# Performance work log

Hardware: AMD Instinct MI355X
Metric: run time of the kernel (lower is better)

The kernel has to match this reference:

```python
import jax, jax.numpy as jnp
import numpy as np

R, T, M, N, L = 128, 4096, 32768, 4096, 16384
ALPHA_LO, ALPHA_HI = 0.01, 1.0
BETA_LO, BETA_HI = 1.0, 8.0


def setup_inputs() -> dict:
    key = jax.random.key(0)
    ks = jax.random.split(key, 7)
    x = jax.random.normal(ks[0], (R, T), dtype=jnp.float32)          # route flows param
    A = jax.random.uniform(ks[1], (M, R), dtype=jnp.float32)          # route->movement incidence
    t0 = jax.random.uniform(ks[2], (L,), dtype=jnp.float32) * 10.0    # free-flow time per c_df row
    cap = jax.random.uniform(ks[3], (L,), dtype=jnp.float32) * 1000.0 + 500.0  # capacity
    radio = jax.random.uniform(ks[4], (L,), dtype=jnp.float32)
    node_ids = jax.random.randint(ks[5], (M,), 0, N, dtype=jnp.int32)  # node of each movement row
    row_node = jax.random.randint(ks[6], (L,), 0, N, dtype=jnp.int32)  # node of each c_df row
    # logit((0.15-0.01)/0.99) and logit((4-1)/7) anchors
    alpha_raw = jnp.float32(np.log(0.141414 / (1 - 0.141414)))
    beta_raw = jnp.float32(np.log((3.0 / 7.0) / (1 - 3.0 / 7.0)))
    return {"x": x, "A": A, "t0": t0, "cap": cap, "radio": radio,
            "alpha_raw": alpha_raw, "beta_raw": beta_raw,
            "node_ids": node_ids, "row_node": row_node}


def reference(x, A, t0, cap, radio, alpha_raw, beta_raw, node_ids, row_node):
    alpha = ALPHA_LO + (ALPHA_HI - ALPHA_LO) * jax.nn.sigmoid(alpha_raw)
    beta = BETA_LO + (BETA_HI - BETA_LO) * jax.nn.sigmoid(beta_raw)
    x_pos = jax.nn.relu(x)                                   # relu(x).clamp(min=0)
    c_pred = A @ x_pos                                        # [M, T]
    # per-node flow: segment-sum of movement rows grouped by node
    node_flow = jax.ops.segment_sum(c_pred, node_ids, num_segments=N)  # [N, T]
    flow = node_flow[row_node]                                # [L, T] gather per c_df row
    ratio = jnp.maximum(flow / cap[:, None], 1e-6)            # (flow/cap).clamp(min=1e-6)
    # y = sum_rows t0*radio + sum_rows t0*alpha*radio * ratio**beta
    y = jnp.sum(t0 * radio) + jnp.einsum("l,lt->t", t0 * alpha * radio, ratio ** beta)
    return (x_pos, c_pred, y)
```

## Files before the change

kernel.cpp:

```cpp
#include <hip/hip_runtime.h>

#define T_DIM 4096
#define R_DIM 128
#define M_DIM 32768
#define N_DIM 4096
#define L_DIM 16384
#define BUCKET_CAP 64

typedef __attribute__((ext_vector_type(8))) short short8;
typedef __attribute__((ext_vector_type(4))) short short4_;
typedef __attribute__((ext_vector_type(4))) float float4_;

__device__ __forceinline__ unsigned short f2bf(float f) {
    unsigned int u = __float_as_uint(f);
    unsigned int r = (u + 0x7fffu + ((u >> 16) & 1u)) >> 16;
    return (unsigned short)r;
}

__global__ __launch_bounds__(256) void prep_x(const float* __restrict__ x,
                                              float* __restrict__ xpos,
                                              unsigned short* __restrict__ Xt) {
    __shared__ unsigned short lds[64][130];
    const int tid = threadIdx.x;
    const int t0 = blockIdx.x * 64;
    #pragma unroll
    for (int it = 0; it < 32; it++) {
        int idx = it * 256 + tid;
        int k = idx >> 6;
        int tt = idx & 63;
        float v = fmaxf(x[k * T_DIM + t0 + tt], 0.0f);
        __builtin_nontemporal_store(v, &xpos[k * T_DIM + t0 + tt]);
        lds[tt][k] = f2bf(v);
    }
    __syncthreads();
    const int w = tid >> 6, lane = tid & 63;
    #pragma unroll
    for (int rep = 0; rep < 16; rep++) {
        int row = w * 16 + rep;
        unsigned int lo = lds[row][2 * lane];
        unsigned int hi = lds[row][2 * lane + 1];
        *(unsigned int*)(Xt + (size_t)(t0 + row) * R_DIM + 2 * lane) = lo | (hi << 16);
    }
}

__global__ __launch_bounds__(256) void cast_A(const float* __restrict__ A,
                                              unsigned short* __restrict__ Ab) {
    size_t id = (size_t)blockIdx.x * 256 + threadIdx.x;
    float4 v0 = *(const float4*)(A + id * 8);
    float4 v1 = *(const float4*)(A + id * 8 + 4);
    short8 b;
    b[0] = (short)f2bf(v0.x); b[1] = (short)f2bf(v0.y);
    b[2] = (short)f2bf(v0.z); b[3] = (short)f2bf(v0.w);
    b[4] = (short)f2bf(v1.x); b[5] = (short)f2bf(v1.y);
    b[6] = (short)f2bf(v1.z); b[7] = (short)f2bf(v1.w);
    *(short8*)(Ab + id * 8) = b;
}

__global__ __launch_bounds__(256) void scatter_nodes(const int* __restrict__ node_ids,
                                                     int* __restrict__ cnt,
                                                     int* __restrict__ bucket) {
    int m = blockIdx.x * 256 + threadIdx.x;
    int n = node_ids[m];
    int slot = atomicAdd(cnt + n, 1);
    if (slot < BUCKET_CAP) bucket[n * BUCKET_CAP + slot] = m;
}

__global__ __launch_bounds__(256) void bseg_gather(const float* __restrict__ A,
                                                   const int* __restrict__ cnt,
                                                   const int* __restrict__ bucket,
                                                   unsigned short* __restrict__ Bb) {
    int n = blockIdx.x * 2 + (threadIdx.x >> 7);
    int k = threadIdx.x & 127;
    int c = cnt[n];
    c = (c > BUCKET_CAP) ? BUCKET_CAP : c;
    float acc = 0.0f;
    for (int s = 0; s < c; s++) {
        int m = bucket[n * BUCKET_CAP + s];
        acc += A[(size_t)m * R_DIM + k];
    }
    Bb[(size_t)n * R_DIM + k] = f2bf(acc);
}

__global__ __launch_bounds__(256) void prep_lw(const float* __restrict__ t0,
                                               const float* __restrict__ cap,
                                               const float* __restrict__ radio,
                                               const float* __restrict__ alpha_raw,
                                               const float* __restrict__ beta_raw,
                                               const int* __restrict__ row_node,
                                               float* __restrict__ gcoef,
                                               float* __restrict__ cterm) {
    int l = blockIdx.x * 256 + threadIdx.x;
    float alpha = 0.01f + 0.99f / (1.0f + expf(-alpha_raw[0]));
    float beta  = 1.0f + 7.0f  / (1.0f + expf(-beta_raw[0]));
    float tv = t0[l], rv = radio[l];
    float rc = 1.0f / cap[l];
    float wv = tv * alpha * rv;
    float g = wv * __builtin_amdgcn_exp2f(beta * __builtin_amdgcn_logf(rc));
    atomicAdd(gcoef + row_node[l], g);
    float p = tv * rv;
    #pragma unroll
    for (int off = 32; off > 0; off >>= 1) p += __shfl_down(p, off, 64);
    if ((threadIdx.x & 63) == 0) atomicAdd(cterm, p);
}

__global__ __launch_bounds__(256) void y_init(const float* __restrict__ cterm,
                                              float* __restrict__ y) {
    int t = blockIdx.x * 256 + threadIdx.x;
    y[t] = cterm[0];
}

__global__ __launch_bounds__(256) void gemm_mfma(const unsigned short* __restrict__ Am,
                                                 const unsigned short* __restrict__ Xt,
                                                 float* __restrict__ C) {
    const int nwg  = gridDim.x * gridDim.y;
    const int orig = blockIdx.y * gridDim.x + blockIdx.x;
    const int cpx  = nwg >> 3;
    const int swz  = (orig & 7) * cpx + (orig >> 3);
    const int bx   = swz & 31;
    const int by   = swz >> 5;

    const int lane = threadIdx.x & 63;
    const int wid  = threadIdx.x >> 6;
    const int quad = lane >> 4;
    const int l16  = lane & 15;
    const int mBase = by * 128 + (wid & 1) * 64;
    const int tBase = bx * 128 + (wid >> 1) * 64;

    float4_ acc[4][4];
    #pragma unroll
    for (int i = 0; i < 4; i++)
        #pragma unroll
        for (int j = 0; j < 4; j++)
            acc[i][j] = (float4_)(0.0f);

    #pragma unroll
    for (int ks = 0; ks < 4; ks++) {
        const int k0 = ks * 32 + quad * 8;
        short8 a[4], b[4];
        #pragma unroll
        for (int i = 0; i < 4; i++) {
            size_t m = (size_t)(mBase + i * 16 + l16);
            a[i] = *(const short8*)(Am + m * R_DIM + k0);
        }
        #pragma unroll
        for (int j = 0; j < 4; j++) {
            size_t t = (size_t)(tBase + j * 16 + l16);
            b[j] = *(const short8*)(Xt + t * R_DIM + k0);
        }
        #pragma unroll
        for (int i = 0; i < 4; i++)
            #pragma unroll
            for (int j = 0; j < 4; j++)
                acc[i][j] = __builtin_amdgcn_mfma_f32_16x16x32_bf16(a[i], b[j], acc[i][j], 0, 0, 0);
    }

    #pragma unroll
    for (int i = 0; i < 4; i++) {
        int row0 = mBase + i * 16 + quad * 4;
        #pragma unroll
        for (int j = 0; j < 4; j++) {
            int col = tBase + j * 16 + l16;
            #pragma unroll
            for (int r = 0; r < 4; r++) {
                __builtin_nontemporal_store(acc[i][j][r], &C[(size_t)(row0 + r) * T_DIM + col]);
            }
        }
    }
}

__global__ __launch_bounds__(256) void gemm_nflow_y(const unsigned short* __restrict__ Bb,
                                                    const unsigned short* __restrict__ Xt,
                                                    const float* __restrict__ gcoef,
                                                    const float* __restrict__ beta_raw,
                                                    float* __restrict__ y) {
    const int nwg  = gridDim.x * gridDim.y;
    const int orig = blockIdx.y * gridDim.x + blockIdx.x;
    const int cpx  = nwg >> 3;
    const int swz  = (orig & 7) * cpx + (orig >> 3);
    const int bx   = swz & 31;
    const int by   = swz >> 5;

    const int lane = threadIdx.x & 63;
    const int wid  = threadIdx.x >> 6;
    const int quad = lane >> 4;
    const int l16  = lane & 15;
    const int bRow  = by * 128;
    const int mBase = bRow + (wid & 1) * 64;
    const int tBase = bx * 128 + (wid >> 1) * 64;

    __shared__ float gc[128];
    if (threadIdx.x < 128) gc[threadIdx.x] = gcoef[bRow + threadIdx.x];

    float4_ acc[4][4];
    #pragma unroll
    for (int i = 0; i < 4; i++)
        #pragma unroll
        for (int j = 0; j < 4; j++)
            acc[i][j] = (float4_)(0.0f);

    #pragma unroll
    for (int ks = 0; ks < 4; ks++) {
        const int k0 = ks * 32 + quad * 8;
        short8 a[4], b[4];
        #pragma unroll
        for (int i = 0; i < 4; i++) {
            size_t m = (size_t)(mBase + i * 16 + l16);
            a[i] = *(const short8*)(Bb + m * R_DIM + k0);
        }
        #pragma unroll
        for (int j = 0; j < 4; j++) {
            size_t t = (size_t)(tBase + j * 16 + l16);
            b[j] = *(const short8*)(Xt + t * R_DIM + k0);
        }
        #pragma unroll
        for (int i = 0; i < 4; i++)
            #pragma unroll
            for (int j = 0; j < 4; j++)
                acc[i][j] = __builtin_amdgcn_mfma_f32_16x16x32_bf16(a[i], b[j], acc[i][j], 0, 0, 0);
    }

    __syncthreads();
    float beta = 1.0f + 7.0f / (1.0f + expf(-beta_raw[0]));
    float p[4] = {0.0f, 0.0f, 0.0f, 0.0f};
    #pragma unroll
    for (int i = 0; i < 4; i++) {
        int r0 = (wid & 1) * 64 + i * 16 + quad * 4;
        #pragma unroll
        for (int r = 0; r < 4; r++) {
            float g = gc[r0 + r];
            #pragma unroll
            for (int j = 0; j < 4; j++) {
                float f = acc[i][j][r];
                float pw = __builtin_amdgcn_exp2f(beta * __builtin_amdgcn_logf(fmaxf(f, 1e-30f)));
                p[j] += g * pw;
            }
        }
    }
    #pragma unroll
    for (int j = 0; j < 4; j++) {
        p[j] += __shfl_xor(p[j], 16, 64);
        p[j] += __shfl_xor(p[j], 32, 64);
        if (quad == 0) atomicAdd(&y[tBase + j * 16 + l16], p[j]);
    }
}

extern "C" void kernel_launch(void* const* d_in, const int* in_sizes, int n_in,
                              void* d_out, int out_size, void* d_ws, size_t ws_size,
                              hipStream_t stream) {
    const float* x         = (const float*)d_in[0];
    const float* A         = (const float*)d_in[1];
    const float* t0        = (const float*)d_in[2];
    const float* cap       = (const float*)d_in[3];
    const float* radio     = (const float*)d_in[4];
    const float* alpha_raw = (const float*)d_in[5];
    const float* beta_raw  = (const float*)d_in[6];
    const int*   node_ids  = (const int*)d_in[7];
    const int*   row_node  = (const int*)d_in[8];

    float* out   = (float*)d_out;
    float* xpos  = out;
    float* cpred = out + (size_t)R_DIM * T_DIM;
    float* y     = cpred + (size_t)M_DIM * T_DIM;

    char* ws = (char*)d_ws;
    unsigned short* Xt     = (unsigned short*)(ws);
    unsigned short* Ab     = (unsigned short*)(ws + (1u << 20));
    unsigned short* Bb     = (unsigned short*)(ws + (9u << 20));
    int*            cnt    = (int*)(ws + (10u << 20));
    float*          gcoef  = (float*)(ws + (10u << 20) + N_DIM * 4);
    float*          csum   = gcoef + N_DIM;
    int*            bucket = (int*)(ws + (11u << 20));

    (void)hipMemsetAsync(cnt, 0, (size_t)(2 * N_DIM + 1) * 4, stream);

    prep_x       <<<dim3(T_DIM / 64), 256, 0, stream>>>(x, xpos, Xt);
    cast_A       <<<dim3((M_DIM * R_DIM / 8) / 256), 256, 0, stream>>>(A, Ab);
    scatter_nodes<<<dim3(M_DIM / 256), 256, 0, stream>>>(node_ids, cnt, bucket);
    prep_lw      <<<dim3(L_DIM / 256), 256, 0, stream>>>(t0, cap, radio, alpha_raw,
                                                         beta_raw, row_node, gcoef, csum);
    y_init       <<<dim3(T_DIM / 256), 256, 0, stream>>>(csum, y);
    bseg_gather  <<<dim3(N_DIM / 2), 256, 0, stream>>>(A, cnt, bucket, Bb);

    gemm_mfma<<<dim3(T_DIM / 128, M_DIM / 128), 256, 0, stream>>>(Ab, Xt, cpred);
    gemm_nflow_y<<<dim3(T_DIM / 128, N_DIM / 128), 256, 0, stream>>>(Bb, Xt, gcoef, beta_raw, y);
}
```

Measured before the change: 647.9 us.

## Fuse A cast into GEMM, merge prep kernels, combine both GEMMs into one launch

Removes the separate cast_A pass and converts A from fp32 to bf16 inside the GEMM's operand load. It merges scatter_nodes with prep_lw, and bseg_gather with y_init, cutting the number of launches. Both GEMMs run in a single grid where the first 1024 blocks do the node-flow/y work and the rest produce c_pred. The c_pred epilogue now transposes results across lanes so each lane writes 16-byte vector stores instead of scalar ones. The cost is twice the A bytes read per GEMM tile plus conversion ALU work and shuffles in the main GEMM.

```diff
diff --git a/kernel.cpp b/kernel.cpp
--- a/kernel.cpp
+++ b/kernel.cpp
@@ -8,7 +8,6 @@
 #define BUCKET_CAP 64
 
 typedef __attribute__((ext_vector_type(8))) short short8;
-typedef __attribute__((ext_vector_type(4))) short short4_;
 typedef __attribute__((ext_vector_type(4))) float float4_;
 
 __device__ __forceinline__ unsigned short f2bf(float f) {
@@ -43,32 +42,46 @@
     }
 }
 
-__global__ __launch_bounds__(256) void cast_A(const float* __restrict__ A,
-                                              unsigned short* __restrict__ Ab) {
-    size_t id = (size_t)blockIdx.x * 256 + threadIdx.x;
-    float4 v0 = *(const float4*)(A + id * 8);
-    float4 v1 = *(const float4*)(A + id * 8 + 4);
-    short8 b;
-    b[0] = (short)f2bf(v0.x); b[1] = (short)f2bf(v0.y);
-    b[2] = (short)f2bf(v0.z); b[3] = (short)f2bf(v0.w);
-    b[4] = (short)f2bf(v1.x); b[5] = (short)f2bf(v1.y);
-    b[6] = (short)f2bf(v1.z); b[7] = (short)f2bf(v1.w);
-    *(short8*)(Ab + id * 8) = b;
-}
-
-__global__ __launch_bounds__(256) void scatter_nodes(const int* __restrict__ node_ids,
-                                                     int* __restrict__ cnt,
-                                                     int* __restrict__ bucket) {
-    int m = blockIdx.x * 256 + threadIdx.x;
-    int n = node_ids[m];
+__global__ __launch_bounds__(256) void prep_scatter(const int* __restrict__ node_ids,
+                                                    int* __restrict__ cnt,
+                                                    int* __restrict__ bucket,
+                                                    const float* __restrict__ t0,
+                                                    const float* __restrict__ cap,
+                                                    const float* __restrict__ radio,
+                                                    const float* __restrict__ alpha_raw,
+                                                    const float* __restrict__ beta_raw,
+                                                    const int* __restrict__ row_node,
+                                                    float* __restrict__ gcoef,
+                                                    float* __restrict__ cterm) {
+    int id = blockIdx.x * 256 + threadIdx.x;
+    int n = node_ids[id];
     int slot = atomicAdd(cnt + n, 1);
-    if (slot < BUCKET_CAP) bucket[n * BUCKET_CAP + slot] = m;
-}
-
-__global__ __launch_bounds__(256) void bseg_gather(const float* __restrict__ A,
-                                                   const int* __restrict__ cnt,
-                                                   const int* __restrict__ bucket,
-                                                   unsigned short* __restrict__ Bb) {
+    if (slot < BUCKET_CAP) bucket[n * BUCKET_CAP + slot] = id;
+    if (id < L_DIM) {
+        float alpha = 0.01f + 0.99f / (1.0f + expf(-alpha_raw[0]));
+        float beta  = 1.0f + 7.0f  / (1.0f + expf(-beta_raw[0]));
+        float tv = t0[id], rv = radio[id];
+        float rc = 1.0f / cap[id];
+        float g = tv * alpha * rv * __builtin_amdgcn_exp2f(beta * __builtin_amdgcn_logf(rc));
+        atomicAdd(gcoef + row_node[id], g);
+        float p = tv * rv;
+        #pragma unroll
+        for (int off = 32; off > 0; off >>= 1) p += __shfl_down(p, off, 64);
+        if ((threadIdx.x & 63) == 0) atomicAdd(cterm, p);
+    }
+}
+
+__global__ __launch_bounds__(256) void bseg_y(const float* __restrict__ A,
+                                              const int* __restrict__ cnt,
+                                              const int* __restrict__ bucket,
+                                              const float* __restrict__ cterm,
+                                              unsigned short* __restrict__ Bb,
+                                              float* __restrict__ y) {
+    if (blockIdx.x >= 2048) {
+        int t = (blockIdx.x - 2048) * 256 + threadIdx.x;
+        y[t] = cterm[0];
+        return;
+    }
     int n = blockIdx.x * 2 + (threadIdx.x >> 7);
     int k = threadIdx.x & 127;
     int c = cnt[n];
@@ -81,166 +94,137 @@
     Bb[(size_t)n * R_DIM + k] = f2bf(acc);
 }
 
-__global__ __launch_bounds__(256) void prep_lw(const float* __restrict__ t0,
-                                               const float* __restrict__ cap,
-                                               const float* __restrict__ radio,
-                                               const float* __restrict__ alpha_raw,
-                                               const float* __restrict__ beta_raw,
-                                               const int* __restrict__ row_node,
-                                               float* __restrict__ gcoef,
-                                               float* __restrict__ cterm) {
-    int l = blockIdx.x * 256 + threadIdx.x;
-    float alpha = 0.01f + 0.99f / (1.0f + expf(-alpha_raw[0]));
-    float beta  = 1.0f + 7.0f  / (1.0f + expf(-beta_raw[0]));
-    float tv = t0[l], rv = radio[l];
-    float rc = 1.0f / cap[l];
-    float wv = tv * alpha * rv;
-    float g = wv * __builtin_amdgcn_exp2f(beta * __builtin_amdgcn_logf(rc));
-    atomicAdd(gcoef + row_node[l], g);
-    float p = tv * rv;
-    #pragma unroll
-    for (int off = 32; off > 0; off >>= 1) p += __shfl_down(p, off, 64);
-    if ((threadIdx.x & 63) == 0) atomicAdd(cterm, p);
-}
-
-__global__ __launch_bounds__(256) void y_init(const float* __restrict__ cterm,
-                                              float* __restrict__ y) {
-    int t = blockIdx.x * 256 + threadIdx.x;
-    y[t] = cterm[0];
-}
-
-__global__ __launch_bounds__(256) void gemm_mfma(const unsigned short* __restrict__ Am,
-                                                 const unsigned short* __restrict__ Xt,
-                                                 float* __restrict__ C) {
-    const int nwg  = gridDim.x * gridDim.y;
-    const int orig = blockIdx.y * gridDim.x + blockIdx.x;
-    const int cpx  = nwg >> 3;
-    const int swz  = (orig & 7) * cpx + (orig >> 3);
-    const int bx   = swz & 31;
-    const int by   = swz >> 5;
-
+__global__ __launch_bounds__(256) void megagemm(const float* __restrict__ A,
+                                                const unsigned short* __restrict__ Bb,
+                                                const unsigned short* __restrict__ Xt,
+                                                const float* __restrict__ gcoef,
+                                                const float* __restrict__ beta_raw,
+                                                float* __restrict__ C,
+                                                float* __restrict__ y) {
+    const int orig = blockIdx.y * 32 + blockIdx.x;
     const int lane = threadIdx.x & 63;
     const int wid  = threadIdx.x >> 6;
     const int quad = lane >> 4;
     const int l16  = lane & 15;
-    const int mBase = by * 128 + (wid & 1) * 64;
-    const int tBase = bx * 128 + (wid >> 1) * 64;
-
-    float4_ acc[4][4];
-    #pragma unroll
-    for (int i = 0; i < 4; i++)
-        #pragma unroll
-        for (int j = 0; j < 4; j++)
-            acc[i][j] = (float4_)(0.0f);
-
-    #pragma unroll
-    for (int ks = 0; ks < 4; ks++) {
-        const int k0 = ks * 32 + quad * 8;
-        short8 a[4], b[4];
+
+    if (orig >= 1024) {
+        const int o2 = orig - 1024;
+        const int s  = (o2 & 7) * 1024 + (o2 >> 3);
+        const int bx = s & 31, by = s >> 5;
+        const int mBase = by * 128 + (wid & 1) * 64;
+        const int tBase = bx * 128 + (wid >> 1) * 64;
+
+        float4_ acc[4][4];
+        #pragma unroll
+        for (int i = 0; i < 4; i++)
+            #pragma unroll
+            for (int j = 0; j < 4; j++)
+                acc[i][j] = (float4_)(0.0f);
+
+        #pragma unroll
+        for (int ks = 0; ks < 4; ks++) {
+            const int k0 = ks * 32 + quad * 8;
+            short8 a[4], b[4];
+            #pragma unroll
+            for (int i = 0; i < 4; i++) {
+                const float* ap = A + (size_t)(mBase + i * 16 + l16) * R_DIM + k0;
+                float4 f0 = *(const float4*)(ap);
+                float4 f1 = *(const float4*)(ap + 4);
+                short8 t;
+                t[0] = (short)f2bf(f0.x); t[1] = (short)f2bf(f0.y);
+                t[2] = (short)f2bf(f0.z); t[3] = (short)f2bf(f0.w);
+                t[4] = (short)f2bf(f1.x); t[5] = (short)f2bf(f1.y);
+                t[6] = (short)f2bf(f1.z); t[7] = (short)f2bf(f1.w);
+                a[i] = t;
+            }
+            #pragma unroll
+            for (int j = 0; j < 4; j++)
+                b[j] = *(const short8*)(Xt + (size_t)(tBase + j * 16 + l16) * R_DIM + k0);
+            #pragma unroll
+            for (int i = 0; i < 4; i++)
+                #pragma unroll
+                for (int j = 0; j < 4; j++)
+                    acc[i][j] = __builtin_amdgcn_mfma_f32_16x16x32_bf16(a[i], b[j], acc[i][j], 0, 0, 0);
+        }
+
         #pragma unroll
         for (int i = 0; i < 4; i++) {
-            size_t m = (size_t)(mBase + i * 16 + l16);
-            a[i] = *(const short8*)(Am + m * R_DIM + k0);
+            #pragma unroll
+            for (int j = 0; j < 4; j++) {
+                float x0 = acc[i][j][0], x1 = acc[i][j][1];
+                float x2 = acc[i][j][2], x3 = acc[i][j][3];
+                float t;
+                t = __shfl_xor((lane & 1) ? x0 : x1, 1, 64);
+                if (lane & 1) x0 = t; else x1 = t;
+                t = __shfl_xor((lane & 1) ? x2 : x3, 1, 64);
+                if (lane & 1) x2 = t; else x3 = t;
+                t = __shfl_xor((lane & 2) ? x0 : x2, 2, 64);
+                if (lane & 2) x0 = t; else x2 = t;
+                t = __shfl_xor((lane & 2) ? x1 : x3, 2, 64);
+                if (lane & 2) x1 = t; else x3 = t;
+                float4_ o; o[0] = x0; o[1] = x1; o[2] = x2; o[3] = x3;
+                int row  = mBase + i * 16 + quad * 4 + (lane & 3);
+                int colb = tBase + j * 16 + (l16 & 12);
+                __builtin_nontemporal_store(o, (float4_*)(C + (size_t)row * T_DIM + colb));
+            }
+        }
+    } else {
+        const int s  = (orig & 7) * 128 + (orig >> 3);
+        const int bx = s & 31, by = s >> 5;
+        const int bRow  = by * 128;
+        const int mBase = bRow + (wid & 1) * 64;
+        const int tBase = bx * 128 + (wid >> 1) * 64;
+
+        __shared__ float gc[128];
+        if (threadIdx.x < 128) gc[threadIdx.x] = gcoef[bRow + threadIdx.x];
+
+        float4_ acc[4][4];
+        #pragma unroll
+        for (int i = 0; i < 4; i++)
+            #pragma unroll
+            for (int j = 0; j < 4; j++)
+                acc[i][j] = (float4_)(0.0f);
+
+        #pragma unroll
+        for (int ks = 0; ks < 4; ks++) {
+            const int k0 = ks * 32 + quad * 8;
+            short8 a[4], b[4];
+            #pragma unroll
+            for (int i = 0; i < 4; i++)
+                a[i] = *(const short8*)(Bb + (size_t)(mBase + i * 16 + l16) * R_DIM + k0);
+            #pragma unroll
+            for (int j = 0; j < 4; j++)
+                b[j] = *(const short8*)(Xt + (size_t)(tBase + j * 16 + l16) * R_DIM + k0);
+            #pragma unroll
+            for (int i = 0; i < 4; i++)
+                #pragma unroll
+                for (int j = 0; j < 4; j++)
+                    acc[i][j] = __builtin_amdgcn_mfma_f32_16x16x32_bf16(a[i], b[j], acc[i][j], 0, 0, 0);
+        }
+
+        __syncthreads();
+        float beta = 1.0f + 7.0f / (1.0f + expf(-beta_raw[0]));
+        float p[4] = {0.0f, 0.0f, 0.0f, 0.0f};
+        #pragma unroll
+        for (int i = 0; i < 4; i++) {
+            int r0 = (wid & 1) * 64 + i * 16 + quad * 4;
+            #pragma unroll
+            for (int r = 0; r < 4; r++) {
+                float g = gc[r0 + r];
+                #pragma unroll
+                for (int j = 0; j < 4; j++) {
+                    float f = acc[i][j][r];
+                    float pw = __builtin_amdgcn_exp2f(beta * __builtin_amdgcn_logf(fmaxf(f, 1e-30f)));
+                    p[j] += g * pw;
+                }
+            }
         }
         #pragma unroll
         for (int j = 0; j < 4; j++) {
-            size_t t = (size_t)(tBase + j * 16 + l16);
-            b[j] = *(const short8*)(Xt + t * R_DIM + k0);
-        }
-        #pragma unroll
-        for (int i = 0; i < 4; i++)
-            #pragma unroll
-            for (int j = 0; j < 4; j++)
-                acc[i][j] = __builtin_amdgcn_mfma_f32_16x16x32_bf16(a[i], b[j], acc[i][j], 0, 0, 0);
-    }
-
-    #pragma unroll
-    for (int i = 0; i < 4; i++) {
-        int row0 = mBase + i * 16 + quad * 4;
-        #pragma unroll
-        for (int j = 0; j < 4; j++) {
-            int col = tBase + j * 16 + l16;
-            #pragma unroll
-            for (int r = 0; r < 4; r++) {
-                __builtin_nontemporal_store(acc[i][j][r], &C[(size_t)(row0 + r) * T_DIM + col]);
-            }
-        }
-    }
-}
-
-__global__ __launch_bounds__(256) void gemm_nflow_y(const unsigned short* __restrict__ Bb,
-                                                    const unsigned short* __restrict__ Xt,
-                                                    const float* __restrict__ gcoef,
-                                                    const float* __restrict__ beta_raw,
-                                                    float* __restrict__ y) {
-    const int nwg  = gridDim.x * gridDim.y;
-    const int orig = blockIdx.y * gridDim.x + blockIdx.x;
-    const int cpx  = nwg >> 3;
-    const int swz  = (orig & 7) * cpx + (orig >> 3);
-    const int bx   = swz & 31;
-    const int by   = swz >> 5;
-
-    const int lane = threadIdx.x & 63;
-    const int wid  = threadIdx.x >> 6;
-    const int quad = lane >> 4;
-    const int l16  = lane & 15;
-    const int bRow  = by * 128;
-    const int mBase = bRow + (wid & 1) * 64;
-    const int tBase = bx * 128 + (wid >> 1) * 64;
-
-    __shared__ float gc[128];
-    if (threadIdx.x < 128) gc[threadIdx.x] = gcoef[bRow + threadIdx.x];
-
-    float4_ acc[4][4];
-    #pragma unroll
-    for (int i = 0; i < 4; i++)
-        #pragma unroll
-        for (int j = 0; j < 4; j++)
-            acc[i][j] = (float4_)(0.0f);
-
-    #pragma unroll
-    for (int ks = 0; ks < 4; ks++) {
-        const int k0 = ks * 32 + quad * 8;
-        short8 a[4], b[4];
-        #pragma unroll
-        for (int i = 0; i < 4; i++) {
-            size_t m = (size_t)(mBase + i * 16 + l16);
-            a[i] = *(const short8*)(Bb + m * R_DIM + k0);
-        }
-        #pragma unroll
-        for (int j = 0; j < 4; j++) {
-            size_t t = (size_t)(tBase + j * 16 + l16);
-            b[j] = *(const short8*)(Xt + t * R_DIM + k0);
-        }
-        #pragma unroll
-        for (int i = 0; i < 4; i++)
-            #pragma unroll
-            for (int j = 0; j < 4; j++)
-                acc[i][j] = __builtin_amdgcn_mfma_f32_16x16x32_bf16(a[i], b[j], acc[i][j], 0, 0, 0);
-    }
-
-    __syncthreads();
-    float beta = 1.0f + 7.0f / (1.0f + expf(-beta_raw[0]));
-    float p[4] = {0.0f, 0.0f, 0.0f, 0.0f};
-    #pragma unroll
-    for (int i = 0; i < 4; i++) {
-        int r0 = (wid & 1) * 64 + i * 16 + quad * 4;
-        #pragma unroll
-        for (int r = 0; r < 4; r++) {
-            float g = gc[r0 + r];
-            #pragma unroll
-            for (int j = 0; j < 4; j++) {
-                float f = acc[i][j][r];
-                float pw = __builtin_amdgcn_exp2f(beta * __builtin_amdgcn_logf(fmaxf(f, 1e-30f)));
-                p[j] += g * pw;
-            }
-        }
-    }
-    #pragma unroll
-    for (int j = 0; j < 4; j++) {
-        p[j] += __shfl_xor(p[j], 16, 64);
-        p[j] += __shfl_xor(p[j], 32, 64);
-        if (quad == 0) atomicAdd(&y[tBase + j * 16 + l16], p[j]);
+            p[j] += __shfl_xor(p[j], 16, 64);
+            p[j] += __shfl_xor(p[j], 32, 64);
+            if (quad == 0) atomicAdd(&y[tBase + j * 16 + l16], p[j]);
+        }
     }
 }
 
@@ -264,23 +248,18 @@
 
     char* ws = (char*)d_ws;
     unsigned short* Xt     = (unsigned short*)(ws);
-    unsigned short* Ab     = (unsigned short*)(ws + (1u << 20));
-    unsigned short* Bb     = (unsigned short*)(ws + (9u << 20));
-    int*            cnt    = (int*)(ws + (10u << 20));
-    float*          gcoef  = (float*)(ws + (10u << 20) + N_DIM * 4);
+    unsigned short* Bb     = (unsigned short*)(ws + (1u << 20));
+    int*            cnt    = (int*)(ws + (2u << 20));
+    float*          gcoef  = (float*)(ws + (2u << 20) + N_DIM * 4);
     float*          csum   = gcoef + N_DIM;
-    int*            bucket = (int*)(ws + (11u << 20));
+    int*            bucket = (int*)(ws + (3u << 20));
 
     (void)hipMemsetAsync(cnt, 0, (size_t)(2 * N_DIM + 1) * 4, stream);
 
-    prep_x       <<<dim3(T_DIM / 64), 256, 0, stream>>>(x, xpos, Xt);
-    cast_A       <<<dim3((M_DIM * R_DIM / 8) / 256), 256, 0, stream>>>(A, Ab);
-    scatter_nodes<<<dim3(M_DIM / 256), 256, 0, stream>>>(node_ids, cnt, bucket);
-    prep_lw      <<<dim3(L_DIM / 256), 256, 0, stream>>>(t0, cap, radio, alpha_raw,
-                                                         beta_raw, row_node, gcoef, csum);
-    y_init       <<<dim3(T_DIM / 256), 256, 0, stream>>>(csum, y);
-    bseg_gather  <<<dim3(N_DIM / 2), 256, 0, stream>>>(A, cnt, bucket, Bb);
-
-    gemm_mfma<<<dim3(T_DIM / 128, M_DIM / 128), 256, 0, stream>>>(Ab, Xt, cpred);
-    gemm_nflow_y<<<dim3(T_DIM / 128, N_DIM / 128), 256, 0, stream>>>(Bb, Xt, gcoef, beta_raw, y);
-}
+    prep_x      <<<dim3(T_DIM / 64), 256, 0, stream>>>(x, xpos, Xt);
+    prep_scatter<<<dim3(M_DIM / 256), 256, 0, stream>>>(node_ids, cnt, bucket,
+                                                        t0, cap, radio, alpha_raw,
+                                                        beta_raw, row_node, gcoef, csum);
+    bseg_y      <<<dim3(2048 + T_DIM / 256), 256, 0, stream>>>(A, cnt, bucket, csum, Bb, y);
+    megagemm    <<<dim3(32, 288), 256, 0, stream>>>(A, Bb, Xt, gcoef, beta_raw, cpred, y);
+}
```

Result: slower. 743.2 us (+14.7%).
